# Kernel tuning notes

Measured on AMD Instinct MI355X. Metric: run time of the kernel, lower is better.

## Reference

```python
import jax, jax.numpy as jnp
import numpy as np

U, D, N, R = 256, 5120, 16, 160  # num_users, d_inner, d_state, dt_rank


def setup_inputs() -> dict:
    key = jax.random.key(0)
    ks = jax.random.split(key, 7)
    s = 0.02
    return {
        "x": jax.random.normal(ks[0], (U, D), jnp.float32),
        "delta_t_proj_w": jax.random.normal(ks[1], (D, R), jnp.float32) * s,
        "dt_proj_w": jax.random.normal(ks[2], (R, D), jnp.float32) * s,
        "dt_proj_b": jax.random.normal(ks[3], (D,), jnp.float32) * s,
        "B_proj_w": jax.random.normal(ks[4], (D, N), jnp.float32) * s,
        "abar": jax.random.uniform(ks[5], (U, D, N), jnp.float32),
        "hidden_state": jax.random.normal(ks[6], (U, D, N), jnp.float32),
    }


def reference(x, delta_t_proj_w, dt_proj_w, dt_proj_b, B_proj_w, abar, hidden_state):
    # delta: [U, D] -- low-rank dt projection then softplus
    dt = jax.nn.softplus(x @ delta_t_proj_w @ dt_proj_w + dt_proj_b)
    # B: [U, N]
    B = x @ B_proj_w
    # bbar[u,i,n] = dt[u,i] * B[u,n]  (discretized B, broadcast over d_inner x d_state)
    bbar = dt[:, :, None] * B[:, None, :]
    # h_new = abar * h + bbar * x   (selective-scan single step)
    h_new = abar * hidden_state + bbar * x[:, :, None]
    return h_new
```

## Files before the change

### kernel.cpp

```cpp
#include <hip/hip_runtime.h>
#include <math.h>

#define U_ 256
#define D_ 5120
#define N_ 16
#define R_ 160
#define J_ 176

#define KB 16
#define NKS 20
#define KSLAB (D_ / NKS)
#define STG (KSLAB / KB)

__device__ __forceinline__ float softplus_f(float v) {
    return v > 20.f ? v : log1pf(__expf(v));
}

__global__ __launch_bounds__(256) void proj_partial(
    const float* __restrict__ x, const float* __restrict__ w1,
    const float* __restrict__ bw, float* __restrict__ P)
{
    const int jt = blockIdx.x;
    const int ks = blockIdx.y;
    const int t  = threadIdx.x;
    const int uq = t & 63;
    const int jq = t >> 6;

    __shared__ float xs[KB][258];
    __shared__ float wsh[KB][16];

    const float* wptr; int ldw, jbase;
    if (jt < 10) { wptr = w1; ldw = R_; jbase = jt * 16; }
    else         { wptr = bw; ldw = N_; jbase = 0; }

    const int k0base = ks * KSLAB;
    const int ux = t >> 2;
    const int cx = t & 3;

    float acc[4][4];
#pragma unroll
    for (int i = 0; i < 4; ++i)
#pragma unroll
        for (int j = 0; j < 4; ++j) acc[i][j] = 0.f;

    float4 xr[4]; float4 wr = make_float4(0.f, 0.f, 0.f, 0.f);

    auto ld = [&](int s, float4 (&xr_)[4], float4& wr_) {
        const int k0 = k0base + s * KB;
#pragma unroll
        for (int i = 0; i < 4; ++i) {
            const int u = ux + i * 64;
            xr_[i] = *(const float4*)&x[u * D_ + k0 + cx * 4];
        }
        if (t < 64) {
            const int k = t >> 2, c = t & 3;
            wr_ = *(const float4*)&wptr[(k0 + k) * ldw + jbase + c * 4];
        }
    };

    ld(0, xr, wr);

    for (int s = 0; s < STG; ++s) {
#pragma unroll
        for (int i = 0; i < 4; ++i) {
            const int u = ux + i * 64;
            xs[cx * 4 + 0][u] = xr[i].x;
            xs[cx * 4 + 1][u] = xr[i].y;
            xs[cx * 4 + 2][u] = xr[i].z;
            xs[cx * 4 + 3][u] = xr[i].w;
        }
        if (t < 64) {
            const int k = t >> 2, c = t & 3;
            *(float4*)&wsh[k][c * 4] = wr;
        }
        __syncthreads();

        float4 xr2[4]; float4 wr2 = make_float4(0.f, 0.f, 0.f, 0.f);
        if (s + 1 < STG) ld(s + 1, xr2, wr2);

#pragma unroll
        for (int kk = 0; kk < KB; ++kk) {
            const float4 wv = *(const float4*)&wsh[kk][jq * 4];
            float xv[4];
#pragma unroll
            for (int i = 0; i < 4; ++i) xv[i] = xs[kk][uq + i * 64];
#pragma unroll
            for (int i = 0; i < 4; ++i) {
                acc[i][0] = fmaf(xv[i], wv.x, acc[i][0]);
                acc[i][1] = fmaf(xv[i], wv.y, acc[i][1]);
                acc[i][2] = fmaf(xv[i], wv.z, acc[i][2]);
                acc[i][3] = fmaf(xv[i], wv.w, acc[i][3]);
            }
        }
        __syncthreads();
        if (s + 1 < STG) {
#pragma unroll
            for (int i = 0; i < 4; ++i) xr[i] = xr2[i];
            wr = wr2;
        }
    }

#pragma unroll
    for (int j = 0; j < 4; ++j) {
        const int jglob = jt * 16 + jq * 4 + j;
        float* row = P + ((size_t)ks * J_ + jglob) * 256;
#pragma unroll
        for (int i = 0; i < 4; ++i) row[uq + i * 64] = acc[i][j];
    }
}

__global__ __launch_bounds__(256) void reduce_kernel(
    const float* __restrict__ P, float* __restrict__ tmpT,
    float* __restrict__ Bm)
{
    const int j = blockIdx.x;
    const int u = threadIdx.x;
    float sum = 0.f;
#pragma unroll
    for (int ks = 0; ks < NKS; ++ks)
        sum += P[((size_t)ks * J_ + j) * 256 + u];
    if (j < R_) tmpT[j * 256 + u] = sum;
    else        Bm[u * N_ + (j - R_)] = sum;
}

__global__ __launch_bounds__(256) void dt_kernel(
    const float* __restrict__ tmpT, const float* __restrict__ w2,
    const float* __restrict__ bias, const float* __restrict__ x,
    float* __restrict__ s)
{
    const int d0 = blockIdx.x * 64;
    const int u0 = blockIdx.y * 64;
    const int t  = threadIdx.x;
    const int uq = t & 15;
    const int dq = t >> 4;

    __shared__ float ts[16][68];
    __shared__ float wls[16][68];

    float acc[4][4];
#pragma unroll
    for (int i = 0; i < 4; ++i)
#pragma unroll
        for (int j = 0; j < 4; ++j) acc[i][j] = 0.f;

    const int rr = t >> 4, cc = t & 15;

    for (int r0 = 0; r0 < R_; r0 += 16) {
        *(float4*)&ts[rr][cc * 4]  = *(const float4*)&tmpT[(r0 + rr) * 256 + u0 + cc * 4];
        *(float4*)&wls[rr][cc * 4] = *(const float4*)&w2[(r0 + rr) * D_ + d0 + cc * 4];
        __syncthreads();
#pragma unroll
        for (int kk = 0; kk < 16; ++kk) {
            const float4 wv = *(const float4*)&wls[kk][dq * 4];
            float av[4];
#pragma unroll
            for (int i = 0; i < 4; ++i) av[i] = ts[kk][uq + i * 16];
#pragma unroll
            for (int i = 0; i < 4; ++i) {
                acc[i][0] = fmaf(av[i], wv.x, acc[i][0]);
                acc[i][1] = fmaf(av[i], wv.y, acc[i][1]);
                acc[i][2] = fmaf(av[i], wv.z, acc[i][2]);
                acc[i][3] = fmaf(av[i], wv.w, acc[i][3]);
            }
        }
        __syncthreads();
    }

    const int d = d0 + dq * 4;
    const float4 bv = *(const float4*)&bias[d];
#pragma unroll
    for (int i = 0; i < 4; ++i) {
        const int u = u0 + uq + 16 * i;
        const float4 xv = *(const float4*)&x[u * D_ + d];
        float4 sv;
        sv.x = softplus_f(acc[i][0] + bv.x) * xv.x;
        sv.y = softplus_f(acc[i][1] + bv.y) * xv.y;
        sv.z = softplus_f(acc[i][2] + bv.z) * xv.z;
        sv.w = softplus_f(acc[i][3] + bv.w) * xv.w;
        *(float4*)&s[u * D_ + d] = sv;
    }
}

__global__ __launch_bounds__(256) void stream_kernel(
    const float* __restrict__ abar, const float* __restrict__ hs,
    const float* __restrict__ s, const float* __restrict__ Bm,
    float* __restrict__ out)
{
    const int u  = blockIdx.y;
    const int bx = blockIdx.x;
    const int t  = threadIdx.x;
    const float4* ab4 = (const float4*)abar;
    const float4* h4  = (const float4*)hs;
    const float4* B4  = (const float4*)Bm;
    float4* o4 = (float4*)out;

    const int ubase = u * (D_ * 4);
    const float* srow = s + u * D_;

#pragma unroll
    for (int k = 0; k < 4; ++k) {
        const int off = bx * 1024 + k * 256 + t;
        const int d   = off >> 2;
        const int n4  = off & 3;
        const int idx = ubase + off;
        const float4 av = ab4[idx];
        const float4 hv = h4[idx];
        const float4 Bv = B4[u * 4 + n4];
        const float  sv = srow[d];
        float4 o;
        o.x = fmaf(av.x, hv.x, sv * Bv.x);
        o.y = fmaf(av.y, hv.y, sv * Bv.y);
        o.z = fmaf(av.z, hv.z, sv * Bv.z);
        o.w = fmaf(av.w, hv.w, sv * Bv.w);
        o4[idx] = o;
    }
}

extern "C" void kernel_launch(void* const* d_in, const int* in_sizes, int n_in,
                              void* d_out, int out_size, void* d_ws, size_t ws_size,
                              hipStream_t stream) {
    const float* x    = (const float*)d_in[0];
    const float* w1   = (const float*)d_in[1];
    const float* w2   = (const float*)d_in[2];
    const float* bias = (const float*)d_in[3];
    const float* bw   = (const float*)d_in[4];
    const float* abar = (const float*)d_in[5];
    const float* hs   = (const float*)d_in[6];
    float* out = (float*)d_out;

    float* P    = (float*)d_ws;
    float* tmpT = P + (size_t)NKS * J_ * 256;
    float* Bm   = tmpT + R_ * 256;
    float* s    = Bm + U_ * N_;

    proj_partial<<<dim3(11, NKS), 256, 0, stream>>>(x, w1, bw, P);
    reduce_kernel<<<dim3(J_), 256, 0, stream>>>(P, tmpT, Bm);
    dt_kernel<<<dim3(80, 4), 256, 0, stream>>>(tmpT, w2, bias, x, s);
    stream_kernel<<<dim3(20, 256), 256, 0, stream>>>(abar, hs, s, Bm, out);
}
```

Measured before the change: 263.3 us.

## Raise split-K, retile dt GEMM, vectorize partial stores, nontemporal stream output

The projection GEMM's split-K count goes from 20 to 64 when the workspace allows it, so the grid is larger, with a fallback to 20 otherwise. Each thread now owns contiguous u rows, so shared-memory reads and partial-sum writes become float4. The dt GEMM is retiled into 64-thread blocks covering 16 users, which quadruples its block count. The streaming kernel batches its loads before computing, hoists the B load out of the loop and uses nontemporal stores for the output. The larger split-K adds more partial-sum traffic to the reduce step, and the smaller dt blocks give less data reuse per block.

```diff
diff --git a/kernel.cpp b/kernel.cpp
--- a/kernel.cpp
+++ b/kernel.cpp
@@ -6,52 +6,48 @@
 #define N_ 16
 #define R_ 160
 #define J_ 176
-
 #define KB 16
-#define NKS 20
-#define KSLAB (D_ / NKS)
-#define STG (KSLAB / KB)
+
+typedef float f4v __attribute__((ext_vector_type(4)));
 
 __device__ __forceinline__ float softplus_f(float v) {
     return v > 20.f ? v : log1pf(__expf(v));
 }
 
+template<int NKS_T>
 __global__ __launch_bounds__(256) void proj_partial(
     const float* __restrict__ x, const float* __restrict__ w1,
     const float* __restrict__ bw, float* __restrict__ P)
 {
+    constexpr int KSLAB_T = D_ / NKS_T;
+    constexpr int STG_T   = KSLAB_T / KB;
+
     const int jt = blockIdx.x;
     const int ks = blockIdx.y;
     const int t  = threadIdx.x;
     const int uq = t & 63;
     const int jq = t >> 6;
 
-    __shared__ float xs[KB][258];
+    __shared__ float xs[KB][260];
     __shared__ float wsh[KB][16];
 
     const float* wptr; int ldw, jbase;
     if (jt < 10) { wptr = w1; ldw = R_; jbase = jt * 16; }
     else         { wptr = bw; ldw = N_; jbase = 0; }
 
-    const int k0base = ks * KSLAB;
+    const int k0base = ks * KSLAB_T;
     const int ux = t >> 2;
     const int cx = t & 3;
 
-    float acc[4][4];
-#pragma unroll
-    for (int i = 0; i < 4; ++i)
-#pragma unroll
-        for (int j = 0; j < 4; ++j) acc[i][j] = 0.f;
+    float acc[4][4] = {};
 
     float4 xr[4]; float4 wr = make_float4(0.f, 0.f, 0.f, 0.f);
 
-    auto ld = [&](int s, float4 (&xr_)[4], float4& wr_) {
-        const int k0 = k0base + s * KB;
-#pragma unroll
-        for (int i = 0; i < 4; ++i) {
-            const int u = ux + i * 64;
-            xr_[i] = *(const float4*)&x[u * D_ + k0 + cx * 4];
-        }
+    auto ld = [&](int s_, float4 (&xr_)[4], float4& wr_) {
+        const int k0 = k0base + s_ * KB;
+#pragma unroll
+        for (int i = 0; i < 4; ++i)
+            xr_[i] = *(const float4*)&x[(ux + i * 64) * D_ + k0 + cx * 4];
         if (t < 64) {
             const int k = t >> 2, c = t & 3;
             wr_ = *(const float4*)&wptr[(k0 + k) * ldw + jbase + c * 4];
@@ -60,7 +56,7 @@
 
     ld(0, xr, wr);
 
-    for (int s = 0; s < STG; ++s) {
+    for (int s = 0; s < STG_T; ++s) {
 #pragma unroll
         for (int i = 0; i < 4; ++i) {
             const int u = ux + i * 64;
@@ -69,31 +65,26 @@
             xs[cx * 4 + 2][u] = xr[i].z;
             xs[cx * 4 + 3][u] = xr[i].w;
         }
-        if (t < 64) {
-            const int k = t >> 2, c = t & 3;
-            *(float4*)&wsh[k][c * 4] = wr;
-        }
+        if (t < 64) *(float4*)&wsh[t >> 2][(t & 3) * 4] = wr;
         __syncthreads();
 
         float4 xr2[4]; float4 wr2 = make_float4(0.f, 0.f, 0.f, 0.f);
-        if (s + 1 < STG) ld(s + 1, xr2, wr2);
+        if (s + 1 < STG_T) ld(s + 1, xr2, wr2);
 
 #pragma unroll
         for (int kk = 0; kk < KB; ++kk) {
             const float4 wv = *(const float4*)&wsh[kk][jq * 4];
-            float xv[4];
-#pragma unroll
-            for (int i = 0; i < 4; ++i) xv[i] = xs[kk][uq + i * 64];
-#pragma unroll
-            for (int i = 0; i < 4; ++i) {
-                acc[i][0] = fmaf(xv[i], wv.x, acc[i][0]);
-                acc[i][1] = fmaf(xv[i], wv.y, acc[i][1]);
-                acc[i][2] = fmaf(xv[i], wv.z, acc[i][2]);
-                acc[i][3] = fmaf(xv[i], wv.w, acc[i][3]);
-            }
-        }
-        __syncthreads();
-        if (s + 1 < STG) {
+            const float4 av = *(const float4*)&xs[kk][uq * 4];
+            const float avx[4] = {av.x, av.y, av.z, av.w};
+            const float wvx[4] = {wv.x, wv.y, wv.z, wv.w};
+#pragma unroll
+            for (int i = 0; i < 4; ++i)
+#pragma unroll
+                for (int j = 0; j < 4; ++j)
+                    acc[i][j] = fmaf(avx[i], wvx[j], acc[i][j]);
+        }
+        __syncthreads();
+        if (s + 1 < STG_T) {
 #pragma unroll
             for (int i = 0; i < 4; ++i) xr[i] = xr2[i];
             wr = wr2;
@@ -102,13 +93,14 @@
 
 #pragma unroll
     for (int j = 0; j < 4; ++j) {
-        const int jglob = jt * 16 + jq * 4 + j;
-        float* row = P + ((size_t)ks * J_ + jglob) * 256;
-#pragma unroll
-        for (int i = 0; i < 4; ++i) row[uq + i * 64] = acc[i][j];
-    }
-}
-
+        float* row = P + ((size_t)ks * J_ + jt * 16 + jq * 4 + j) * 256;
+        float4 v;
+        v.x = acc[0][j]; v.y = acc[1][j]; v.z = acc[2][j]; v.w = acc[3][j];
+        *(float4*)&row[uq * 4] = v;
+    }
+}
+
+template<int NKS_T>
 __global__ __launch_bounds__(256) void reduce_kernel(
     const float* __restrict__ P, float* __restrict__ tmpT,
     float* __restrict__ Bm)
@@ -116,52 +108,52 @@
     const int j = blockIdx.x;
     const int u = threadIdx.x;
     float sum = 0.f;
-#pragma unroll
-    for (int ks = 0; ks < NKS; ++ks)
+#pragma unroll 8
+    for (int ks = 0; ks < NKS_T; ++ks)
         sum += P[((size_t)ks * J_ + j) * 256 + u];
     if (j < R_) tmpT[j * 256 + u] = sum;
     else        Bm[u * N_ + (j - R_)] = sum;
 }
 
-__global__ __launch_bounds__(256) void dt_kernel(
+__global__ __launch_bounds__(64) void dt_kernel(
     const float* __restrict__ tmpT, const float* __restrict__ w2,
     const float* __restrict__ bias, const float* __restrict__ x,
     float* __restrict__ s)
 {
     const int d0 = blockIdx.x * 64;
-    const int u0 = blockIdx.y * 64;
+    const int u0 = blockIdx.y * 16;
     const int t  = threadIdx.x;
-    const int uq = t & 15;
-    const int dq = t >> 4;
-
-    __shared__ float ts[16][68];
-    __shared__ float wls[16][68];
-
-    float acc[4][4];
-#pragma unroll
-    for (int i = 0; i < 4; ++i)
-#pragma unroll
-        for (int j = 0; j < 4; ++j) acc[i][j] = 0.f;
-
-    const int rr = t >> 4, cc = t & 15;
-
-    for (int r0 = 0; r0 < R_; r0 += 16) {
-        *(float4*)&ts[rr][cc * 4]  = *(const float4*)&tmpT[(r0 + rr) * 256 + u0 + cc * 4];
-        *(float4*)&wls[rr][cc * 4] = *(const float4*)&w2[(r0 + rr) * D_ + d0 + cc * 4];
-        __syncthreads();
-#pragma unroll
-        for (int kk = 0; kk < 16; ++kk) {
-            const float4 wv = *(const float4*)&wls[kk][dq * 4];
-            float av[4];
-#pragma unroll
-            for (int i = 0; i < 4; ++i) av[i] = ts[kk][uq + i * 16];
-#pragma unroll
-            for (int i = 0; i < 4; ++i) {
-                acc[i][0] = fmaf(av[i], wv.x, acc[i][0]);
-                acc[i][1] = fmaf(av[i], wv.y, acc[i][1]);
-                acc[i][2] = fmaf(av[i], wv.z, acc[i][2]);
-                acc[i][3] = fmaf(av[i], wv.w, acc[i][3]);
-            }
+    const int du = t & 3;
+    const int dd = t >> 4 == 0 ? (t >> 2) : (t >> 2);
+    const int dq = t >> 2;
+
+    __shared__ float ts[KB][16];
+    __shared__ float ws_[KB][68];
+
+    float acc[4][4] = {};
+
+    const int rT = t >> 2, cT = t & 3;
+    const int rw = t & 15, cw = t >> 4;
+
+    for (int r0 = 0; r0 < R_; r0 += KB) {
+        *(float4*)&ts[rT][cT * 4] =
+            *(const float4*)&tmpT[(r0 + rT) * 256 + u0 + cT * 4];
+#pragma unroll
+        for (int q = 0; q < 4; ++q)
+            *(float4*)&ws_[rw][(cw + q * 4) * 4] =
+                *(const float4*)&w2[(r0 + rw) * D_ + d0 + (cw + q * 4) * 4];
+        __syncthreads();
+#pragma unroll
+        for (int kk = 0; kk < KB; ++kk) {
+            const float4 av = *(const float4*)&ts[kk][du * 4];
+            const float4 wv = *(const float4*)&ws_[kk][dq * 4];
+            const float avx[4] = {av.x, av.y, av.z, av.w};
+            const float wvx[4] = {wv.x, wv.y, wv.z, wv.w};
+#pragma unroll
+            for (int i = 0; i < 4; ++i)
+#pragma unroll
+                for (int j = 0; j < 4; ++j)
+                    acc[i][j] = fmaf(avx[i], wvx[j], acc[i][j]);
         }
         __syncthreads();
     }
@@ -170,7 +162,7 @@
     const float4 bv = *(const float4*)&bias[d];
 #pragma unroll
     for (int i = 0; i < 4; ++i) {
-        const int u = u0 + uq + 16 * i;
+        const int u = u0 + du * 4 + i;
         const float4 xv = *(const float4*)&x[u * D_ + d];
         float4 sv;
         sv.x = softplus_f(acc[i][0] + bv.x) * xv.x;
@@ -189,30 +181,30 @@
     const int u  = blockIdx.y;
     const int bx = blockIdx.x;
     const int t  = threadIdx.x;
-    const float4* ab4 = (const float4*)abar;
-    const float4* h4  = (const float4*)hs;
-    const float4* B4  = (const float4*)Bm;
-    float4* o4 = (float4*)out;
-
-    const int ubase = u * (D_ * 4);
+    const float4* __restrict__ ab4 = (const float4*)abar;
+    const float4* __restrict__ h4  = (const float4*)hs;
+    f4v* o4 = (f4v*)out;
+
     const float* srow = s + u * D_;
-
+    const float4 Bv = ((const float4*)Bm)[u * 4 + (t & 3)];
+    const int base = u * (D_ * 4) + bx * 1024 + t;
+
+    float4 av[4], hv[4];
+    float  sv[4];
+#pragma unroll
+    for (int k = 0; k < 4; ++k) av[k] = ab4[base + k * 256];
+#pragma unroll
+    for (int k = 0; k < 4; ++k) hv[k] = h4[base + k * 256];
+#pragma unroll
+    for (int k = 0; k < 4; ++k) sv[k] = srow[(bx * 1024 + k * 256 + t) >> 2];
 #pragma unroll
     for (int k = 0; k < 4; ++k) {
-        const int off = bx * 1024 + k * 256 + t;
-        const int d   = off >> 2;
-        const int n4  = off & 3;
-        const int idx = ubase + off;
-        const float4 av = ab4[idx];
-        const float4 hv = h4[idx];
-        const float4 Bv = B4[u * 4 + n4];
-        const float  sv = srow[d];
-        float4 o;
-        o.x = fmaf(av.x, hv.x, sv * Bv.x);
-        o.y = fmaf(av.y, hv.y, sv * Bv.y);
-        o.z = fmaf(av.z, hv.z, sv * Bv.z);
-        o.w = fmaf(av.w, hv.w, sv * Bv.w);
-        o4[idx] = o;
+        f4v o;
+        o.x = fmaf(av[k].x, hv[k].x, sv[k] * Bv.x);
+        o.y = fmaf(av[k].y, hv[k].y, sv[k] * Bv.y);
+        o.z = fmaf(av[k].z, hv[k].z, sv[k] * Bv.z);
+        o.w = fmaf(av[k].w, hv[k].w, sv[k] * Bv.w);
+        __builtin_nontemporal_store(o, &o4[base + k * 256]);
     }
 }
 
@@ -228,13 +220,24 @@
     const float* hs   = (const float*)d_in[6];
     float* out = (float*)d_out;
 
-    float* P    = (float*)d_ws;
-    float* tmpT = P + (size_t)NKS * J_ * 256;
-    float* Bm   = tmpT + R_ * 256;
-    float* s    = Bm + U_ * N_;
-
-    proj_partial<<<dim3(11, NKS), 256, 0, stream>>>(x, w1, bw, P);
-    reduce_kernel<<<dim3(J_), 256, 0, stream>>>(P, tmpT, Bm);
-    dt_kernel<<<dim3(80, 4), 256, 0, stream>>>(tmpT, w2, bias, x, s);
+    float* P = (float*)d_ws;
+    const size_t need64 = ((size_t)64 * J_ * 256 + (size_t)R_ * 256 +
+                           (size_t)U_ * N_ + (size_t)U_ * D_) * sizeof(float);
+
+    float *tmpT, *Bm, *s;
+    if (ws_size >= need64) {
+        tmpT = P + (size_t)64 * J_ * 256;
+        Bm   = tmpT + R_ * 256;
+        s    = Bm + U_ * N_;
+        proj_partial<64><<<dim3(11, 64), 256, 0, stream>>>(x, w1, bw, P);
+        reduce_kernel<64><<<dim3(J_), 256, 0, stream>>>(P, tmpT, Bm);
+    } else {
+        tmpT = P + (size_t)20 * J_ * 256;
+        Bm   = tmpT + R_ * 256;
+        s    = Bm + U_ * N_;
+        proj_partial<20><<<dim3(11, 20), 256, 0, stream>>>(x, w1, bw, P);
+        reduce_kernel<20><<<dim3(J_), 256, 0, stream>>>(P, tmpT, Bm);
+    }
+    dt_kernel<<<dim3(80, 16), 64, 0, stream>>>(tmpT, w2, bias, x, s);
     stream_kernel<<<dim3(20, 256), 256, 0, stream>>>(abar, hs, s, Bm, out);
 }
```

Result: no change. 261.0 us (-0.9%).
